# Optimization experiments

Hardware: AMD Instinct MI355X
Metric: run time of the kernel (lower is better)

## Reference

```python
import jax, jax.numpy as jnp
import numpy as np

WEIGHT = 0.1
N_BINS = 64
EPS = 1e-08  # fp32: max(base_eps, 1e-8)


def setup_inputs() -> dict:
    key = jax.random.key(0)
    k1, k2 = jax.random.split(key)
    pred = jax.random.normal(k1, (16, 1, 512, 512), dtype=jnp.float32)
    target = jax.random.normal(k2, (16, 1, 512, 512), dtype=jnp.float32)
    return {"pred": pred, "target": target}


def _soft_hist(x_norm, bin_centers, bin_width):
    # x_norm: [B, N]; bin_centers: [n_bins]
    # Gaussian kernel density -> sum over N -> [B, n_bins]
    diff = x_norm[:, :, None] - bin_centers[None, None, :]  # [B, N, n_bins]
    kern = jnp.exp(-(diff ** 2) / (2.0 * bin_width ** 2))
    return kern.sum(axis=1)


def reference(pred, target):
    B = pred.shape[0]
    pred_flat = pred.reshape(B, -1)
    target_flat = target.reshape(B, -1)

    vmin = target_flat.min(axis=-1, keepdims=True)
    vmax = target_flat.max(axis=-1, keepdims=True)

    bin_edges = jnp.linspace(0.0, 1.0, N_BINS + 1, dtype=pred.dtype)
    bin_centers = (bin_edges[:-1] + bin_edges[1:]) / 2
    bin_width = bin_edges[1] - bin_edges[0]

    denom = vmax - vmin + EPS
    pred_norm = (pred_flat - vmin) / denom
    target_norm = (target_flat - vmin) / denom

    pred_hist = _soft_hist(pred_norm, bin_centers, bin_width)      # [B, n_bins]
    target_hist = _soft_hist(target_norm, bin_centers, bin_width)  # [B, n_bins]

    pred_prob = pred_hist / (pred_hist.sum(axis=-1, keepdims=True) + EPS)
    target_prob = target_hist / (target_hist.sum(axis=-1, keepdims=True) + EPS)

    kl = target_prob * (jnp.log(target_prob + EPS) - jnp.log(pred_prob + EPS))
    return WEIGHT * kl.sum(axis=-1).mean()
```

## Files before the change

kernel.cpp:

```cpp
#include <hip/hip_runtime.h>
#include <math.h>

#define NB    16
#define NPB   (512*512)
#define NBINS 64
#define MMB   16
#define CB    64
#define EPSF  1e-8f
#define QF    0.84932180517f
#define L2E   1.44269504089f
#define INV_E 0.36787944117f
#define LN2   0.69314718056f


__global__ __launch_bounds__(256) void minmax_k(const float4* __restrict__ tgt,
                                                float* __restrict__ mmn,
                                                float* __restrict__ mmx,
                                                float* __restrict__ hist) {
    const int batch = blockIdx.x >> 4, sub = blockIdx.x & 15;
    if (sub == 0 && threadIdx.x < 128) {
        const int tens = threadIdx.x >> 6, lane = threadIdx.x & 63;
        hist[(tens * NB + batch) * NBINS + lane] = 0.0f;
    }

    const int F4 = NPB / 4 / MMB;
    const float4* p = tgt + (size_t)batch * (NPB / 4) + (size_t)sub * F4;
    float mn = 3.4e38f, mx = -3.4e38f;
    for (int i = threadIdx.x; i < F4; i += 256) {
        float4 v = p[i];
        mn = fminf(mn, fminf(fminf(v.x, v.y), fminf(v.z, v.w)));
        mx = fmaxf(mx, fmaxf(fmaxf(v.x, v.y), fmaxf(v.z, v.w)));
    }
    #pragma unroll
    for (int o = 1; o < 64; o <<= 1) {
        mn = fminf(mn, __shfl_xor(mn, o));
        mx = fmaxf(mx, __shfl_xor(mx, o));
    }
    __shared__ float smn[4], smx[4];
    const int wave = threadIdx.x >> 6, lane = threadIdx.x & 63;
    if (lane == 0) { smn[wave] = mn; smx[wave] = mx; }
    __syncthreads();
    if (threadIdx.x == 0) {
        mmn[blockIdx.x] = fminf(fminf(smn[0], smn[1]), fminf(smn[2], smn[3]));
        mmx[blockIdx.x] = fmaxf(fmaxf(smx[0], smx[1]), fmaxf(smx[2], smx[3]));
    }
}

__global__ __launch_bounds__(256, 8) void hist_k(const float4* __restrict__ pred,
                                                 const float4* __restrict__ tgt,
                                                 const float* __restrict__ mmn,
                                                 const float* __restrict__ mmx,
                                                 float* __restrict__ hist) {
    const int blk   = blockIdx.x;
    const int tens  = blk & 1;
    const int batch = (blk >> 1) & (NB - 1);
    const int chunk = blk >> 5;
    const int wave  = threadIdx.x >> 6, lane = threadIdx.x & 63;
    const int kbase = 16 * wave;

    const int F4C = NPB / 4 / CB;
    const float4* __restrict__ src = (tens ? tgt : pred)
        + (size_t)batch * (NPB / 4) + (size_t)chunk * F4C;

    float4 v = src[lane];

    float vmin = mmn[batch * MMB], vmax = mmx[batch * MMB];
    #pragma unroll
    for (int i = 1; i < MMB; ++i) {
        vmin = fminf(vmin, mmn[batch * MMB + i]);
        vmax = fmaxf(vmax, mmx[batch * MMB + i]);
    }
    const float s64 = 64.0f / (vmax - vmin + EPSF);
    const float b0  = fmaf(-vmin, s64, -0.5f);
    const float gb  = -((float)kbase + 0.5f) * L2E;

    float acc[16];
    #pragma unroll
    for (int k = 0; k < 16; ++k) acc[k] = 0.0f;

    const int NIT = F4C / 64;
    #pragma unroll 1
    for (int it = 0; it < NIT; ++it) {
        float4 vn = src[(it < NIT - 1 ? (it + 1) * 64 : 0) + lane];
        float u0 = fmaf(v.x, s64, b0), u1 = fmaf(v.y, s64, b0);
        float u2 = fmaf(v.z, s64, b0), u3 = fmaf(v.w, s64, b0);
        float q0 = u0 * QF, q1 = u1 * QF, q2 = u2 * QF, q3 = u3 * QF;
        float G0 = __builtin_amdgcn_exp2f(fmaf(u0, L2E, gb));
        float G1 = __builtin_amdgcn_exp2f(fmaf(u1, L2E, gb));
        float G2 = __builtin_amdgcn_exp2f(fmaf(u2, L2E, gb));
        float G3 = __builtin_amdgcn_exp2f(fmaf(u3, L2E, gb));
        #pragma unroll
        for (int j = 0; j < 2; ++j) {
            const float c = (float)(kbase + 8 * j) * QF;
            float d0 = q0 - c, d1 = q1 - c, d2 = q2 - c, d3 = q3 - c;
            float E0 = __builtin_amdgcn_exp2f(-(d0 * d0));
            float E1 = __builtin_amdgcn_exp2f(-(d1 * d1));
            float E2 = __builtin_amdgcn_exp2f(-(d2 * d2));
            float E3 = __builtin_amdgcn_exp2f(-(d3 * d3));
            #pragma unroll
            for (int i = 0; i < 8; ++i) {
                acc[8 * j + i] += (E0 + E1) + (E2 + E3);
                E0 *= G0; E1 *= G1; E2 *= G2; E3 *= G3;
                G0 *= INV_E; G1 *= INV_E; G2 *= INV_E; G3 *= INV_E;
            }
        }
        v = vn;
    }

    float keep = 0.0f;
    #pragma unroll
    for (int i = 0; i < 16; ++i) {
        float t = acc[i];
        #pragma unroll
        for (int o = 1; o < 64; o <<= 1) t += __shfl_xor(t, o);
        if (lane == i) keep = t;
    }
    if (lane < 16)
        unsafeAtomicAdd(&hist[(tens * NB + batch) * NBINS + kbase + lane], keep);
}

__global__ __launch_bounds__(256) void final_k(const float* __restrict__ hist,
                                               float* __restrict__ out) {
    const int lane = threadIdx.x & 63, wave = threadIdx.x >> 6;
    __shared__ float wacc[4];
    float a = 0.0f;
    for (int b = wave; b < NB; b += 4) {
        float hp = hist[b * NBINS + lane];
        float ht = hist[(NB + b) * NBINS + lane];
        float sp = hp, st = ht;
        #pragma unroll
        for (int o = 1; o < 64; o <<= 1) {
            sp += __shfl_xor(sp, o);
            st += __shfl_xor(st, o);
        }
        float pp = hp / (sp + EPSF);
        float pt = ht / (st + EPSF);
        float term = pt * ((__builtin_amdgcn_logf(pt + EPSF)
                          - __builtin_amdgcn_logf(pp + EPSF)) * LN2);
        #pragma unroll
        for (int o = 1; o < 64; o <<= 1) term += __shfl_xor(term, o);
        a += term;
    }
    if (lane == 0) wacc[wave] = a;
    __syncthreads();
    if (threadIdx.x == 0)
        out[0] = 0.1f * (wacc[0] + wacc[1] + wacc[2] + wacc[3]) / (float)NB;
}

extern "C" void kernel_launch(void* const* d_in, const int* in_sizes, int n_in,
                              void* d_out, int out_size, void* d_ws, size_t ws_size,
                              hipStream_t stream) {
    const float* pred = (const float*)d_in[0];
    const float* tgt  = (const float*)d_in[1];
    float* mmn  = (float*)d_ws;
    float* mmx  = mmn + NB * MMB;
    float* hist = mmx + NB * MMB;
    float* out  = (float*)d_out;

    minmax_k<<<NB * MMB, 256, 0, stream>>>((const float4*)tgt, mmn, mmx, hist);
    hist_k  <<<2 * NB * CB, 256, 0, stream>>>((const float4*)pred, (const float4*)tgt,
                                              mmn, mmx, hist);
    final_k <<<1, 256, 0, stream>>>(hist, out);
}
```

Before: 122.2 us.

## Recompute Gaussian bins from a single center with per-bin constant factors

New measurement: 115.4 us. -5.5%, faster.

```diff
diff --git a/kernel.cpp b/kernel.cpp
--- a/kernel.cpp
+++ b/kernel.cpp
@@ -4,20 +4,20 @@
 #define NB    16
 #define NPB   (512*512)
 #define NBINS 64
-#define MMB   16
+#define MMB   64
 #define CB    64
 #define EPSF  1e-8f
 #define QF    0.84932180517f
 #define L2E   1.44269504089f
-#define INV_E 0.36787944117f
 #define LN2   0.69314718056f
+#define RCLMP 1e30f
 
 
 __global__ __launch_bounds__(256) void minmax_k(const float4* __restrict__ tgt,
                                                 float* __restrict__ mmn,
                                                 float* __restrict__ mmx,
                                                 float* __restrict__ hist) {
-    const int batch = blockIdx.x >> 4, sub = blockIdx.x & 15;
+    const int batch = blockIdx.x / MMB, sub = blockIdx.x % MMB;
     if (sub == 0 && threadIdx.x < 128) {
         const int tens = threadIdx.x >> 6, lane = threadIdx.x & 63;
         hist[(tens * NB + batch) * NBINS + lane] = 0.0f;
@@ -26,8 +26,9 @@
     const int F4 = NPB / 4 / MMB;
     const float4* p = tgt + (size_t)batch * (NPB / 4) + (size_t)sub * F4;
     float mn = 3.4e38f, mx = -3.4e38f;
-    for (int i = threadIdx.x; i < F4; i += 256) {
-        float4 v = p[i];
+    #pragma unroll
+    for (int i = 0; i < F4 / 256; ++i) {
+        float4 v = p[i * 256 + threadIdx.x];
         mn = fminf(mn, fminf(fminf(v.x, v.y), fminf(v.z, v.w)));
         mx = fmaxf(mx, fmaxf(fmaxf(v.x, v.y), fmaxf(v.z, v.w)));
     }
@@ -64,45 +65,56 @@
 
     float4 v = src[lane];
 
-    float vmin = mmn[batch * MMB], vmax = mmx[batch * MMB];
+    float vmin = mmn[batch * MMB + lane];
+    float vmax = mmx[batch * MMB + lane];
     #pragma unroll
-    for (int i = 1; i < MMB; ++i) {
-        vmin = fminf(vmin, mmn[batch * MMB + i]);
-        vmax = fmaxf(vmax, mmx[batch * MMB + i]);
+    for (int o = 1; o < 64; o <<= 1) {
+        vmin = fminf(vmin, __shfl_xor(vmin, o));
+        vmax = fmaxf(vmax, __shfl_xor(vmax, o));
     }
     const float s64 = 64.0f / (vmax - vmin + EPSF);
-    const float b0  = fmaf(-vmin, s64, -0.5f);
-    const float gb  = -((float)kbase + 0.5f) * L2E;
+    const float bk8 = fmaf(-vmin, s64, -0.5f) - (float)(kbase + 8);
 
     float acc[16];
     #pragma unroll
     for (int k = 0; k < 16; ++k) acc[k] = 0.0f;
 
+    const float C1 = 0.60653065971f,   C2 = 0.13533528324f,
+                C3 = 0.01110899654f,   C4 = 3.35462627903e-4f,
+                C5 = 3.72665317208e-6f, C6 = 1.52299797447e-8f,
+                C7 = 2.28973484833e-11f, C8 = 1.26641655490e-14f;
+
     const int NIT = F4C / 64;
     #pragma unroll 1
     for (int it = 0; it < NIT; ++it) {
         float4 vn = src[(it < NIT - 1 ? (it + 1) * 64 : 0) + lane];
-        float u0 = fmaf(v.x, s64, b0), u1 = fmaf(v.y, s64, b0);
-        float u2 = fmaf(v.z, s64, b0), u3 = fmaf(v.w, s64, b0);
-        float q0 = u0 * QF, q1 = u1 * QF, q2 = u2 * QF, q3 = u3 * QF;
-        float G0 = __builtin_amdgcn_exp2f(fmaf(u0, L2E, gb));
-        float G1 = __builtin_amdgcn_exp2f(fmaf(u1, L2E, gb));
-        float G2 = __builtin_amdgcn_exp2f(fmaf(u2, L2E, gb));
-        float G3 = __builtin_amdgcn_exp2f(fmaf(u3, L2E, gb));
         #pragma unroll
-        for (int j = 0; j < 2; ++j) {
-            const float c = (float)(kbase + 8 * j) * QF;
-            float d0 = q0 - c, d1 = q1 - c, d2 = q2 - c, d3 = q3 - c;
-            float E0 = __builtin_amdgcn_exp2f(-(d0 * d0));
-            float E1 = __builtin_amdgcn_exp2f(-(d1 * d1));
-            float E2 = __builtin_amdgcn_exp2f(-(d2 * d2));
-            float E3 = __builtin_amdgcn_exp2f(-(d3 * d3));
-            #pragma unroll
-            for (int i = 0; i < 8; ++i) {
-                acc[8 * j + i] += (E0 + E1) + (E2 + E3);
-                E0 *= G0; E1 *= G1; E2 *= G2; E3 *= G3;
-                G0 *= INV_E; G1 *= INV_E; G2 *= INV_E; G3 *= INV_E;
-            }
+        for (int pq = 0; pq < 4; ++pq) {
+            float xin = (pq == 0) ? v.x : (pq == 1) ? v.y : (pq == 2) ? v.z : v.w;
+            float d  = fmaf(xin, s64, bk8);
+            float x  = d * L2E;
+            float r  = fminf(__builtin_amdgcn_exp2f(x),  RCLMP);
+            float ri = fminf(__builtin_amdgcn_exp2f(-x), RCLMP);
+            float t  = d * QF;
+            float A  = __builtin_amdgcn_exp2f(-(t * t));
+            float T = A;
+            acc[8] += A;
+            T *= r;  acc[9]  = fmaf(T, C1, acc[9]);
+            T *= r;  acc[10] = fmaf(T, C2, acc[10]);
+            T *= r;  acc[11] = fmaf(T, C3, acc[11]);
+            T *= r;  acc[12] = fmaf(T, C4, acc[12]);
+            T *= r;  acc[13] = fmaf(T, C5, acc[13]);
+            T *= r;  acc[14] = fmaf(T, C6, acc[14]);
+            T *= r;  acc[15] = fmaf(T, C7, acc[15]);
+            float U = A;
+            U *= ri; acc[7] = fmaf(U, C1, acc[7]);
+            U *= ri; acc[6] = fmaf(U, C2, acc[6]);
+            U *= ri; acc[5] = fmaf(U, C3, acc[5]);
+            U *= ri; acc[4] = fmaf(U, C4, acc[4]);
+            U *= ri; acc[3] = fmaf(U, C5, acc[3]);
+            U *= ri; acc[2] = fmaf(U, C6, acc[2]);
+            U *= ri; acc[1] = fmaf(U, C7, acc[1]);
+            U *= ri; acc[0] = fmaf(U, C8, acc[0]);
         }
         v = vn;
     }
```
